# Kernel optimization log

Measured on AMD Instinct MI355X. Metric: run time of the kernel, lower is better.

The kernel has to match this reference:

```python
import jax, jax.numpy as jnp
import numpy as np

D_MODEL = 1024
NUM_HEADS = 16
D_K = D_MODEL // NUM_HEADS
BATCH = 8
SEQ = 1024


def setup_inputs() -> dict:
    key = jax.random.key(0)
    ks = jax.random.split(key, 16)
    s = 1.0 / np.sqrt(D_MODEL)
    def lin(i):
        W = jax.random.uniform(ks[i], (D_MODEL, D_MODEL), jnp.float32, -s, s)
        b = jax.random.uniform(ks[i + 1], (D_MODEL,), jnp.float32, -s, s)
        return W, b
    Wq, bq = lin(0)
    Wk, bk = lin(2)
    Wv, bv = lin(4)
    Wg, bg = lin(6)
    Wbeta, bbeta = lin(8)
    Wo, bo = lin(10)
    X = jax.random.normal(ks[12], (BATCH, SEQ, D_MODEL), jnp.float32)
    Y = jax.random.normal(ks[13], (BATCH, SEQ, D_MODEL), jnp.float32)
    return dict(X=X, Y=Y, Wq=Wq, bq=bq, Wk=Wk, bk=bk, Wv=Wv, bv=bv,
                Wg=Wg, bg=bg, Wbeta=Wbeta, bbeta=bbeta, Wo=Wo, bo=bo)


def _split_heads(x):
    b, s, _ = x.shape
    return x.reshape(b, s, NUM_HEADS, D_K).transpose(0, 2, 1, 3)  # [b,h,s,d_k]


def _attend(q_in, kv_in, Wq, bq, Wk, bk, Wv, bv, Wg, bg, Wbeta, bbeta, Wo, bo):
    Q = _split_heads(q_in @ Wq + bq)
    K = _split_heads(kv_in @ Wk + bk)
    V = _split_heads(kv_in @ Wv + bv)
    scores = jnp.einsum('bhqd,bhkd->bhqk', Q, K) / jnp.sqrt(jnp.float32(D_K))
    attn = jax.nn.softmax(scores, axis=-1)
    ctx = jnp.einsum('bhqk,bhkd->bhqd', attn, V)
    b, h, s, d = ctx.shape
    ctx = ctx.transpose(0, 2, 1, 3).reshape(b, s, h * d)
    out = (ctx @ Wg + bg) * jnp.sqrt(jnp.float32(D_K)) + (ctx @ Wbeta + bbeta)
    return out @ Wo + bo


def reference(X, Y, Wq, bq, Wk, bk, Wv, bv, Wg, bg, Wbeta, bbeta, Wo, bo):
    params = (Wq, bq, Wk, bk, Wv, bv, Wg, bg, Wbeta, bbeta, Wo, bo)
    Y_new = _attend(X, Y, *params)   # pass 1: queries from X, keys/values from Y
    X_new = _attend(Y_new, X, *params)  # pass 2: queries from new Y, kv from original X
    return (X_new, Y_new)
```

## Files before the change

kernel.cpp:

```cpp
#include <hip/hip_runtime.h>

typedef unsigned short u16;
typedef __bf16 bf16x8 __attribute__((ext_vector_type(8)));
typedef float f32x4 __attribute__((ext_vector_type(4)));
typedef float f32x16 __attribute__((ext_vector_type(16)));
typedef u16 u16x4 __attribute__((ext_vector_type(4)));
typedef unsigned int u32x4v __attribute__((ext_vector_type(4)));

#define LOG2E_OVER_8 0.18033688011112043f

__device__ __forceinline__ u16 f2bf(float f) {
  union { float f; unsigned int u; } x{f};
  unsigned int r = (x.u + 0x7fffu + ((x.u >> 16) & 1u)) >> 16;
  return (u16)r;
}

__device__ __forceinline__ float bf2f(u16 v) {
  union { unsigned int u; float f; } x;
  x.u = ((unsigned int)v) << 16;
  return x.f;
}

__device__ __forceinline__ unsigned cvtpk(float a, float b) {
  unsigned r;
  asm("v_cvt_pk_bf16_f32 %0, %1, %2" : "=v"(r) : "v"(a), "v"(b));
  return r;
}

__device__ __forceinline__ void gld16(const void* g, void* l) {
  __builtin_amdgcn_global_load_lds((const __attribute__((address_space(1))) unsigned int*)g,
                                   (__attribute__((address_space(3))) unsigned int*)l,
                                   16, 0, 0);
}

__global__ void prep_w(const float* __restrict__ Wq, const float* __restrict__ Wk,
                       const float* __restrict__ Wv, const float* __restrict__ Wg,
                       const float* __restrict__ Wb, const float* __restrict__ Wo,
                       u16* __restrict__ Wqt, u16* __restrict__ Wkt, u16* __restrict__ Wvt,
                       u16* __restrict__ Wcn, u16* __restrict__ Wot)
{
  __shared__ float tile[32][33];
  const int m = blockIdx.z;
  const int nb = blockIdx.x * 32, kb = blockIdx.y * 32;
  const int tx = threadIdx.x, ty = threadIdx.y;
  const float* src = (m == 0) ? Wq : (m == 1) ? Wk : (m == 2) ? Wv : (m == 3) ? Wg : Wo;
  u16* dst = (m == 0) ? Wqt : (m == 1) ? Wkt : (m == 2) ? Wvt : (m == 3) ? Wcn : Wot;
#pragma unroll
  for (int i = 0; i < 4; ++i) {
    const int k = kb + ty + i * 8;
    float v = src[k * 1024 + nb + tx];
    if (m == 3) v = 8.0f * v + Wb[k * 1024 + nb + tx];
    if (m == 0) v *= LOG2E_OVER_8;
    if (m == 3) dst[k * 1024 + nb + tx] = f2bf(v);
    else        tile[ty + i * 8][tx] = v;
  }
  __syncthreads();
  if (m != 3) {
#pragma unroll
    for (int i = 0; i < 4; ++i) {
      const int r = ty + i * 8;
      dst[(nb + r) * 1024 + kb + tx] = f2bf(tile[tx][r]);
    }
  }
}

__global__ void prep_b(const float* __restrict__ bq, const float* __restrict__ bg,
                       const float* __restrict__ bb,
                       float* __restrict__ bqs, float* __restrict__ bcs)
{
  const int i = blockIdx.x * 256 + threadIdx.x;
  if (i < 1024) {
    bqs[i] = bq[i] * LOG2E_OVER_8;
    bcs[i] = 8.0f * bg[i] + bb[i];
  }
}

__global__ void cvt2_bf16(const float* __restrict__ in0, u16* __restrict__ out0,
                          const float* __restrict__ in1, u16* __restrict__ out1, int n)
{
  int i = (blockIdx.x * blockDim.x + threadIdx.x) * 4;
  const int stride = gridDim.x * blockDim.x * 4;
  for (; i < n; i += stride) {
    const float4 v0 = *reinterpret_cast<const float4*>(in0 + i);
    u16x4 o0;
    o0.x = f2bf(v0.x); o0.y = f2bf(v0.y); o0.z = f2bf(v0.z); o0.w = f2bf(v0.w);
    *reinterpret_cast<u16x4*>(out0 + i) = o0;
    const float4 v1 = *reinterpret_cast<const float4*>(in1 + i);
    u16x4 o1;
    o1.x = f2bf(v1.x); o1.y = f2bf(v1.y); o1.z = f2bf(v1.z); o1.w = f2bf(v1.w);
    *reinterpret_cast<u16x4*>(out1 + i) = o1;
  }
}

template<int EPI, int NB>
__device__ __forceinline__ void gemm_body(int bid0, u16* lA, u16* lB,
                                          const u16* __restrict__ A,
                                          const u16* __restrict__ Bt,
                                          const float* __restrict__ bias,
                                          u16* __restrict__ outb, float* __restrict__ outf)
{
  int bid = (bid0 & 7) * NB + (bid0 >> 3);
  const int row0 = (bid >> 3) * 128;
  const int col0 = (bid & 7) * 128;
  const int t = threadIdx.x;
  const int w = t >> 6, lane = t & 63;
  const int l15 = lane & 15, l4 = lane >> 4;
  const int wr = w >> 1, wc = w & 1;
  const int l7 = l15 & 7;

  const u16* gA[4];
  const u16* gB[4];
#pragma unroll
  for (int k2 = 0; k2 < 4; ++k2) {
    const int c = k2 * 256 + t;
    const int r = c >> 3;
    const int sc = ((c & 7) ^ (r & 7)) * 8;
    gA[k2] = A + (row0 + r) * 1024 + sc;
    gB[k2] = Bt + (col0 + r) * 1024 + sc;
  }

  f32x4 acc[4][4] = {};

  for (int kt = 0; kt < 1024; kt += 64) {
#pragma unroll
    for (int k2 = 0; k2 < 4; ++k2) {
      gld16(gA[k2] + kt, lA + (k2 * 256 + w * 64) * 8);
      gld16(gB[k2] + kt, lB + (k2 * 256 + w * 64) * 8);
    }
    __syncthreads();
    bf16x8 aF[4][2], bF[4][2];
#pragma unroll
    for (int m = 0; m < 4; ++m)
#pragma unroll
      for (int ks = 0; ks < 2; ++ks)
        aF[m][ks] = *reinterpret_cast<const bf16x8*>(
            &lA[(wr * 64 + m * 16 + l15) * 64 + ((ks * 4 + l4) ^ l7) * 8]);
#pragma unroll
    for (int n = 0; n < 4; ++n)
#pragma unroll
      for (int ks = 0; ks < 2; ++ks)
        bF[n][ks] = *reinterpret_cast<const bf16x8*>(
            &lB[(wc * 64 + n * 16 + l15) * 64 + ((ks * 4 + l4) ^ l7) * 8]);
#pragma unroll
    for (int m = 0; m < 4; ++m)
#pragma unroll
      for (int n = 0; n < 4; ++n) {
        acc[m][n] = __builtin_amdgcn_mfma_f32_16x16x32_bf16(aF[m][0], bF[n][0], acc[m][n], 0, 0, 0);
        acc[m][n] = __builtin_amdgcn_mfma_f32_16x16x32_bf16(aF[m][1], bF[n][1], acc[m][n], 0, 0, 0);
      }
    __syncthreads();
  }

  float bv[4];
#pragma unroll
  for (int n = 0; n < 4; ++n)
    bv[n] = (EPI == 4) ? 0.0f : bias[col0 + wc * 64 + n * 16 + l15];
#pragma unroll
  for (int m = 0; m < 4; ++m) {
#pragma unroll
    for (int n = 0; n < 4; ++n) {
      const int c = col0 + wc * 64 + n * 16 + l15;
#pragma unroll
      for (int j = 0; j < 4; ++j) {
        const int r = row0 + wr * 64 + m * 16 + l4 * 4 + j;
        const float v = acc[m][n][j] + bv[n];
        if constexpr (EPI == 0 || EPI == 4) {
          outb[r * 1024 + c] = f2bf(v);
        } else if constexpr (EPI == 1) {
          outf[r * 1024 + c] = v;
          outb[r * 1024 + c] = f2bf(v);
        } else if constexpr (EPI == 2) {
          const int bi = r >> 10, s = r & 1023;
          const int h = c >> 6, d = c & 63;
          outb[((bi * 16 + h) * 64 + d) * 1024 + s] = f2bf(v);
        } else {
          outf[r * 1024 + c] = v;
        }
      }
    }
  }
}

__device__ __forceinline__ void bias_body(int bb, const float* __restrict__ bcs,
                                          const u16* __restrict__ Wot,
                                          const float* __restrict__ bo,
                                          float* __restrict__ bco)
{
  const int t = threadIdx.x, w = t >> 6, l = t & 63;
  const int n = bb * 4 + w;
  const u16* row = Wot + n * 1024;
  float a = 0.f;
#pragma unroll
  for (int i = 0; i < 16; ++i) a += bcs[l + 64 * i] * bf2f(row[l + 64 * i]);
#pragma unroll
  for (int d = 1; d < 64; d <<= 1) a += __shfl_xor(a, d);
  if (l == 0) bco[n] = a + bo[n];
}

template<int EPI, int NB = 64>
__global__ __launch_bounds__(256, 3)
void gemm_k(const u16* __restrict__ A, const u16* __restrict__ Bt,
            const float* __restrict__ bias,
            u16* __restrict__ outb, float* __restrict__ outf)
{
  __shared__ u16 lA[128 * 64];
  __shared__ u16 lB[128 * 64];
  gemm_body<EPI, NB>((int)blockIdx.x, lA, lB, A, Bt, bias, outb, outf);
}

__global__ __launch_bounds__(256, 3)
void gemm3_k(const u16* __restrict__ A0, const u16* __restrict__ B0,
             const float* __restrict__ c0, u16* __restrict__ o0,
             const u16* __restrict__ A1, const u16* __restrict__ B1,
             const float* __restrict__ c1, u16* __restrict__ o1,
             const u16* __restrict__ A2, const u16* __restrict__ B2,
             const float* __restrict__ c2, u16* __restrict__ o2,
             const u16* __restrict__ A3, const u16* __restrict__ B3,
             u16* __restrict__ o3,
             const float* __restrict__ bcs, const float* __restrict__ bo,
             float* __restrict__ bco)
{
  __shared__ u16 lA[128 * 64];
  __shared__ u16 lB[128 * 64];
  const int id = (int)blockIdx.x;
  if (id < 512)       gemm_body<0, 64>(id,        lA, lB, A0, B0, c0, o0, nullptr);
  else if (id < 1024) gemm_body<0, 64>(id - 512,  lA, lB, A1, B1, c1, o1, nullptr);
  else if (id < 1536) gemm_body<2, 64>(id - 1024, lA, lB, A2, B2, c2, o2, nullptr);
  else if (id < 1600) gemm_body<4, 8>(id - 1536,  lA, lB, A3, B3, nullptr, o3, nullptr);
  else                bias_body(id - 1600, bcs, A3, bo, bco);
}

__global__ __launch_bounds__(256, 4)
void attn_k(const u16* __restrict__ Q, const u16* __restrict__ K,
            const u16* __restrict__ Vt, const u16* __restrict__ ctx_unused,
            u16* __restrict__ ctx)
{
  __shared__ u16 lK[64 * 72];
  __shared__ u16 lV[64 * 72];
  __shared__ float lsumI[4][32];
  const int id = (int)blockIdx.x;
  const int xcd = id & 7, o = id >> 3;
  const int pair = xcd * 16 + (o >> 3);
  const int qt = o & 7;
  const int b = pair >> 4, h = pair & 15;
  const int t = threadIdx.x, w = t >> 6, lane = t & 63;
  const int l31 = lane & 31, hi = lane >> 5;
  const int q0 = qt * 128 + w * 32;
  const u16* Qp = Q + (size_t)b * (1024 * 1024) + h * 64;
  const u16* Kp = K + (size_t)b * (1024 * 1024) + h * 64;
  const u16* Vp = Vt + (size_t)(b * 16 + h) * (64 * 1024);

  const int r0 = t >> 3, c0 = (t & 7) * 8;

  bf16x8 bQ[4];
#pragma unroll
  for (int ks = 0; ks < 4; ++ks)
    bQ[ks] = *reinterpret_cast<const bf16x8*>(&Qp[(q0 + l31) * 1024 + ks * 16 + hi * 8]);

  f32x16 acc[2] = {};
  float lsum = 0.f;

  bf16x8 sK0, sK1, sV0, sV1;
  sK0 = *reinterpret_cast<const bf16x8*>(&Kp[(r0) * 1024 + c0]);
  sK1 = *reinterpret_cast<const bf16x8*>(&Kp[(r0 + 32) * 1024 + c0]);
  sV0 = *reinterpret_cast<const bf16x8*>(&Vp[r0 * 1024 + c0]);
  sV1 = *reinterpret_cast<const bf16x8*>(&Vp[(r0 + 32) * 1024 + c0]);

  for (int it = 0; it < 16; ++it) {
    const int kv0 = it * 64;
    __syncthreads();
    *reinterpret_cast<bf16x8*>(&lK[r0 * 72 + c0]) = sK0;
    *reinterpret_cast<bf16x8*>(&lK[(r0 + 32) * 72 + c0]) = sK1;
    *reinterpret_cast<bf16x8*>(&lV[r0 * 72 + c0]) = sV0;
    *reinterpret_cast<bf16x8*>(&lV[(r0 + 32) * 72 + c0]) = sV1;
    __syncthreads();
    if (it + 1 < 16) {
      const int nk = kv0 + 64;
      sK0 = *reinterpret_cast<const bf16x8*>(&Kp[(nk + r0) * 1024 + c0]);
      sK1 = *reinterpret_cast<const bf16x8*>(&Kp[(nk + r0 + 32) * 1024 + c0]);
      sV0 = *reinterpret_cast<const bf16x8*>(&Vp[r0 * 1024 + nk + c0]);
      sV1 = *reinterpret_cast<const bf16x8*>(&Vp[(r0 + 32) * 1024 + nk + c0]);
    }

    f32x16 sS[2] = {};
    __builtin_amdgcn_s_setprio(1);
#pragma unroll
    for (int tt = 0; tt < 2; ++tt) {
#pragma unroll
      for (int ks = 0; ks < 4; ++ks) {
        const bf16x8 aK = *reinterpret_cast<const bf16x8*>(
            &lK[(tt * 32 + l31) * 72 + ks * 16 + hi * 8]);
        sS[tt] = __builtin_amdgcn_mfma_f32_32x32x16_bf16(aK, bQ[ks], sS[tt], 0, 0, 0);
      }
    }
    __builtin_amdgcn_s_setprio(0);

    unsigned pa[2][2][4];
#pragma unroll
    for (int tt = 0; tt < 2; ++tt) {
      float p[16];
      float s0 = 0.f, s1 = 0.f, s2 = 0.f, s3 = 0.f;
#pragma unroll
      for (int r = 0; r < 16; r += 4) {
        p[r]     = __builtin_amdgcn_exp2f(sS[tt][r]);
        p[r + 1] = __builtin_amdgcn_exp2f(sS[tt][r + 1]);
        p[r + 2] = __builtin_amdgcn_exp2f(sS[tt][r + 2]);
        p[r + 3] = __builtin_amdgcn_exp2f(sS[tt][r + 3]);
        s0 += p[r]; s1 += p[r + 1]; s2 += p[r + 2]; s3 += p[r + 3];
      }
      lsum += (s0 + s1) + (s2 + s3);
      unsigned wv[8];
#pragma unroll
      for (int i = 0; i < 8; ++i) wv[i] = cvtpk(p[2 * i], p[2 * i + 1]);
#pragma unroll
      for (int c = 0; c < 2; ++c) {
        unsigned a0 = wv[4 * c + 0], b0 = wv[4 * c + 2];
        unsigned a1 = wv[4 * c + 1], b1 = wv[4 * c + 3];
        asm("v_permlane32_swap_b32 %0, %1" : "+v"(a0), "+v"(b0));
        asm("v_permlane32_swap_b32 %0, %1" : "+v"(a1), "+v"(b1));
        pa[tt][c][0] = a0;
        pa[tt][c][1] = a1;
        pa[tt][c][2] = b0;
        pa[tt][c][3] = b1;
      }
    }

    __builtin_amdgcn_s_setprio(1);
#pragma unroll
    for (int tt = 0; tt < 2; ++tt)
#pragma unroll
      for (int c = 0; c < 2; ++c) {
        u32x4v pw;
        pw.x = pa[tt][c][0]; pw.y = pa[tt][c][1];
        pw.z = pa[tt][c][2]; pw.w = pa[tt][c][3];
        const bf16x8 aP = __builtin_bit_cast(bf16x8, pw);
#pragma unroll
        for (int dt = 0; dt < 2; ++dt) {
          const bf16x8 bV = *reinterpret_cast<const bf16x8*>(
              &lV[(dt * 32 + l31) * 72 + tt * 32 + c * 16 + hi * 8]);
          acc[dt] = __builtin_amdgcn_mfma_f32_32x32x16_bf16(aP, bV, acc[dt], 0, 0, 0);
        }
      }
    __builtin_amdgcn_s_setprio(0);
  }

  const float ltot = lsum + __shfl_xor(lsum, 32);
  if (hi == 0) lsumI[w][l31] = 1.0f / ltot;
  u16* Cp = ctx + (size_t)b * (1024 * 1024) + h * 64;
#pragma unroll
  for (int dt = 0; dt < 2; ++dt)
#pragma unroll
    for (int r = 0; r < 16; ++r) {
      const int q = (r & 3) + 8 * (r >> 2) + 4 * hi;
      const float inv = lsumI[w][q];
      Cp[(q0 + q) * 1024 + dt * 32 + l31] = f2bf(acc[dt][r] * inv);
    }
}

extern "C" void kernel_launch(void* const* d_in, const int* in_sizes, int n_in,
                              void* d_out, int out_size, void* d_ws, size_t ws_size,
                              hipStream_t stream)
{
  (void)in_sizes; (void)n_in; (void)out_size; (void)ws_size;
  const float* X  = (const float*)d_in[0];
  const float* Y  = (const float*)d_in[1];
  const float* Wq = (const float*)d_in[2];
  const float* bq = (const float*)d_in[3];
  const float* Wk = (const float*)d_in[4];
  const float* bk = (const float*)d_in[5];
  const float* Wv = (const float*)d_in[6];
  const float* bv = (const float*)d_in[7];
  const float* Wg = (const float*)d_in[8];
  const float* bg = (const float*)d_in[9];
  const float* Wb = (const float*)d_in[10];
  const float* bb = (const float*)d_in[11];
  const float* Wo = (const float*)d_in[12];
  const float* bo = (const float*)d_in[13];
  float* out = (float*)d_out;
  char* ws = (char*)d_ws;
  const size_t MB = 1024ull * 1024ull;

  u16* Wqt = (u16*)(ws + 0 * MB);
  u16* Wkt = (u16*)(ws + 2 * MB);
  u16* Wvt = (u16*)(ws + 4 * MB);
  u16* Wcn = (u16*)(ws + 6 * MB);
  u16* Wot = (u16*)(ws + 8 * MB);
  u16* Wcot = (u16*)(ws + 10 * MB);
  u16* Xb = (u16*)(ws + 12 * MB);
  u16* Yb = (u16*)(ws + 28 * MB);
  u16* Qb = (u16*)(ws + 44 * MB);
  u16* Kb = (u16*)(ws + 60 * MB);
  u16* Vt = (u16*)(ws + 76 * MB);
  u16* Cx = (u16*)(ws + 92 * MB);
  float* bqs = (float*)(ws + 108 * MB);
  float* bcs = (float*)(ws + 108 * MB + 4096);
  float* bco = (float*)(ws + 108 * MB + 8192);
  const int NEL = 8 * 1024 * 1024;

  prep_w<<<dim3(32, 32, 5), dim3(32, 8), 0, stream>>>(Wq, Wk, Wv, Wg, Wb, Wo,
                                                      Wqt, Wkt, Wvt, Wcn, Wot);
  prep_b<<<4, 256, 0, stream>>>(bq, bg, bb, bqs, bcs);
  cvt2_bf16<<<2048, 256, 0, stream>>>(X, Xb, Y, Yb, NEL);

  gemm3_k<<<1856, 256, 0, stream>>>(Xb, Wqt, bqs, Qb,
                                    Yb, Wkt, bk, Kb,
                                    Yb, Wvt, bv, Vt,
                                    Wot, Wcn, Wcot,
                                    bcs, bo, bco);
  attn_k<<<dim3(1024), 256, 0, stream>>>(Qb, Kb, Vt, nullptr, Cx);
  gemm_k<1><<<512, 256, 0, stream>>>(Cx, Wcot, bco, Yb, out + NEL);

  gemm3_k<<<1536, 256, 0, stream>>>(Yb, Wqt, bqs, Qb,
                                    Xb, Wkt, bk, Kb,
                                    Xb, Wvt, bv, Vt,
                                    nullptr, nullptr, nullptr,
                                    nullptr, nullptr, nullptr);
  attn_k<<<dim3(1024), 256, 0, stream>>>(Qb, Kb, Vt, nullptr, Cx);
  gemm_k<3><<<512, 256, 0, stream>>>(Cx, Wcot, bco, nullptr, out);
}
```

Before: 283.3 us.

## Overlap pass-2 K/V projections with pass-1 attention in one fused launch

Pass 2's K and V projections depend only on X, so they are moved into a combined kernel that runs them alongside pass-1 attention. Separate K/V buffers in extra workspace hold the results, leaving only the Q projection to run after pass 1 finishes. The aim is to fill idle compute units during attention and remove a serialization point. Occupancy hints on the GEMM kernels drop from 3 to 2 blocks per SU, and the fused kernel mixes attention and GEMM blocks with different resource needs, which may lower attention occupancy. The new path only runs when the workspace is at least 143 MB, otherwise the old sequence is used.

```diff
diff --git a/kernel.cpp b/kernel.cpp
--- a/kernel.cpp
+++ b/kernel.cpp
@@ -198,7 +198,7 @@
 }
 
 template<int EPI, int NB = 64>
-__global__ __launch_bounds__(256, 3)
+__global__ __launch_bounds__(256, 2)
 void gemm_k(const u16* __restrict__ A, const u16* __restrict__ Bt,
             const float* __restrict__ bias,
             u16* __restrict__ outb, float* __restrict__ outf)
@@ -208,7 +208,7 @@
   gemm_body<EPI, NB>((int)blockIdx.x, lA, lB, A, Bt, bias, outb, outf);
 }
 
-__global__ __launch_bounds__(256, 3)
+__global__ __launch_bounds__(256, 2)
 void gemm3_k(const u16* __restrict__ A0, const u16* __restrict__ B0,
              const float* __restrict__ c0, u16* __restrict__ o0,
              const u16* __restrict__ A1, const u16* __restrict__ B1,
@@ -230,15 +230,12 @@
   else                bias_body(id - 1600, bcs, A3, bo, bco);
 }
 
-__global__ __launch_bounds__(256, 4)
-void attn_k(const u16* __restrict__ Q, const u16* __restrict__ K,
-            const u16* __restrict__ Vt, const u16* __restrict__ ctx_unused,
-            u16* __restrict__ ctx)
-{
-  __shared__ u16 lK[64 * 72];
-  __shared__ u16 lV[64 * 72];
-  __shared__ float lsumI[4][32];
-  const int id = (int)blockIdx.x;
+__device__ __forceinline__ void attn_body(int id, u16* lK, u16* lV, float* lsumI,
+                                          const u16* __restrict__ Q,
+                                          const u16* __restrict__ K,
+                                          const u16* __restrict__ Vt,
+                                          u16* __restrict__ ctx)
+{
   const int xcd = id & 7, o = id >> 3;
   const int pair = xcd * 16 + (o >> 3);
   const int qt = o & 7;
@@ -345,23 +342,53 @@
   }
 
   const float ltot = lsum + __shfl_xor(lsum, 32);
-  if (hi == 0) lsumI[w][l31] = 1.0f / ltot;
+  if (hi == 0) lsumI[w * 32 + l31] = 1.0f / ltot;
   u16* Cp = ctx + (size_t)b * (1024 * 1024) + h * 64;
 #pragma unroll
   for (int dt = 0; dt < 2; ++dt)
 #pragma unroll
     for (int r = 0; r < 16; ++r) {
       const int q = (r & 3) + 8 * (r >> 2) + 4 * hi;
-      const float inv = lsumI[w][q];
+      const float inv = lsumI[w * 32 + q];
       Cp[(q0 + q) * 1024 + dt * 32 + l31] = f2bf(acc[dt][r] * inv);
     }
+}
+
+__global__ __launch_bounds__(256, 4)
+void attn_k(const u16* __restrict__ Q, const u16* __restrict__ K,
+            const u16* __restrict__ Vt, u16* __restrict__ ctx)
+{
+  __shared__ u16 lK[64 * 72];
+  __shared__ u16 lV[64 * 72];
+  __shared__ float lsumI[4 * 32];
+  attn_body((int)blockIdx.x, lK, lV, lsumI, Q, K, Vt, ctx);
+}
+
+__global__ __launch_bounds__(256, 2)
+void attn_kv_k(const u16* __restrict__ Q, const u16* __restrict__ K,
+               const u16* __restrict__ Vt, u16* __restrict__ ctx,
+               const u16* __restrict__ A1, const u16* __restrict__ B1,
+               const float* __restrict__ c1, u16* __restrict__ o1,
+               const u16* __restrict__ A2, const u16* __restrict__ B2,
+               const float* __restrict__ c2, u16* __restrict__ o2)
+{
+  __shared__ __align__(16) char smem[32768];
+  const int id = (int)blockIdx.x;
+  if (id < 1024) {
+    attn_body(id, (u16*)smem, (u16*)(smem + 9216), (float*)(smem + 18432),
+              Q, K, Vt, ctx);
+  } else if (id < 1536) {
+    gemm_body<0, 64>(id - 1024, (u16*)smem, (u16*)(smem + 16384), A1, B1, c1, o1, nullptr);
+  } else {
+    gemm_body<2, 64>(id - 1536, (u16*)smem, (u16*)(smem + 16384), A2, B2, c2, o2, nullptr);
+  }
 }
 
 extern "C" void kernel_launch(void* const* d_in, const int* in_sizes, int n_in,
                               void* d_out, int out_size, void* d_ws, size_t ws_size,
                               hipStream_t stream)
 {
-  (void)in_sizes; (void)n_in; (void)out_size; (void)ws_size;
+  (void)in_sizes; (void)n_in; (void)out_size;
   const float* X  = (const float*)d_in[0];
   const float* Y  = (const float*)d_in[1];
   const float* Wq = (const float*)d_in[2];
@@ -395,7 +422,10 @@
   float* bqs = (float*)(ws + 108 * MB);
   float* bcs = (float*)(ws + 108 * MB + 4096);
   float* bco = (float*)(ws + 108 * MB + 8192);
+  u16* Kb2 = (u16*)(ws + 110 * MB);
+  u16* Vt2 = (u16*)(ws + 126 * MB);
   const int NEL = 8 * 1024 * 1024;
+  const bool overlap = ws_size >= 143 * MB;
 
   prep_w<<<dim3(32, 32, 5), dim3(32, 8), 0, stream>>>(Wq, Wk, Wv, Wg, Wb, Wo,
                                                       Wqt, Wkt, Wvt, Wcn, Wot);
@@ -407,14 +437,22 @@
                                     Yb, Wvt, bv, Vt,
                                     Wot, Wcn, Wcot,
                                     bcs, bo, bco);
-  attn_k<<<dim3(1024), 256, 0, stream>>>(Qb, Kb, Vt, nullptr, Cx);
-  gemm_k<1><<<512, 256, 0, stream>>>(Cx, Wcot, bco, Yb, out + NEL);
-
-  gemm3_k<<<1536, 256, 0, stream>>>(Yb, Wqt, bqs, Qb,
-                                    Xb, Wkt, bk, Kb,
-                                    Xb, Wvt, bv, Vt,
-                                    nullptr, nullptr, nullptr,
-                                    nullptr, nullptr, nullptr);
-  attn_k<<<dim3(1024), 256, 0, stream>>>(Qb, Kb, Vt, nullptr, Cx);
+  if (overlap) {
+    attn_kv_k<<<2048, 256, 0, stream>>>(Qb, Kb, Vt, Cx,
+                                        Xb, Wkt, bk, Kb2,
+                                        Xb, Wvt, bv, Vt2);
+    gemm_k<1><<<512, 256, 0, stream>>>(Cx, Wcot, bco, Yb, out + NEL);
+    gemm_k<0><<<512, 256, 0, stream>>>(Yb, Wqt, bqs, Qb, nullptr);
+    attn_k<<<1024, 256, 0, stream>>>(Qb, Kb2, Vt2, Cx);
+  } else {
+    attn_k<<<1024, 256, 0, stream>>>(Qb, Kb, Vt, Cx);
+    gemm_k<1><<<512, 256, 0, stream>>>(Cx, Wcot, bco, Yb, out + NEL);
+    gemm3_k<<<1536, 256, 0, stream>>>(Yb, Wqt, bqs, Qb,
+                                      Xb, Wkt, bk, Kb,
+                                      Xb, Wvt, bv, Vt,
+                                      nullptr, nullptr, nullptr,
+                                      nullptr, nullptr, nullptr);
+    attn_k<<<1024, 256, 0, stream>>>(Qb, Kb, Vt, Cx);
+  }
   gemm_k<3><<<512, 256, 0, stream>>>(Cx, Wcot, bco, nullptr, out);
 }
```

Measured after the change: 292.0 us. 3.1% more time.
